# Kernel tuning notes

Measured on AMD Instinct MI355X. Metric: run time of the kernel, lower is better.

## Reference

```python
import jax, jax.numpy as jnp
import numpy as np

E = 1024  # embed_dim
H = 16    # num_heads
D = E // H  # head_dim


def setup_inputs() -> dict:
    key = jax.random.key(0)
    ks = jax.random.split(key, 9)
    s = 0.02
    return {
        "hidden_state": jax.random.normal(ks[0], (4, 1024, E), jnp.float32),
        "Wq": jax.random.normal(ks[1], (H, D, E), jnp.float32) * s,
        "bq": jax.random.normal(ks[2], (H, D), jnp.float32) * s,
        "Wk": jax.random.normal(ks[3], (H, D, E), jnp.float32) * s,
        "bk": jax.random.normal(ks[4], (H, D), jnp.float32) * s,
        "Wv": jax.random.normal(ks[5], (H, D, E), jnp.float32) * s,
        "bv": jax.random.normal(ks[6], (H, D), jnp.float32) * s,
        "Wo": jax.random.normal(ks[7], (E, E), jnp.float32) * s,
        "bo": jax.random.normal(ks[8], (E,), jnp.float32) * s,
    }


def _mha(x, Wq, bq, Wk, bk, Wv, bv, Wo, bo):
    # Per-head linear projections (torch Linear: y = x W^T + b), batched over heads.
    q = jnp.einsum("bse,hde->bhsd", x, Wq) + bq[None, :, None, :]
    k = jnp.einsum("bse,hde->bhsd", x, Wk) + bk[None, :, None, :]
    v = jnp.einsum("bse,hde->bhsd", x, Wv) + bv[None, :, None, :]
    scores = jnp.einsum("bhsd,bhtd->bhst", q, k) / jnp.sqrt(jnp.asarray(D, x.dtype))
    w = jax.nn.softmax(scores, axis=-1)  # F.softmax default -> last dim
    o = jnp.einsum("bhst,bhtd->bhsd", w, v)
    # concat heads along last dim: [B,S,H*D] in head order (matches torch.cat)
    B, _, S, _ = o.shape
    o = jnp.transpose(o, (0, 2, 1, 3)).reshape(B, S, H * D)
    return o @ Wo.T + bo


def reference(hidden_state, Wq, bq, Wk, bk, Wv, bv, Wo, bo):
    return _mha(hidden_state, Wq, bq, Wk, bk, Wv, bv, Wo, bo)
```

## Files before the change

kernel.cpp:

```cpp
#include <hip/hip_runtime.h>
#include <hip/hip_bf16.h>
#include <stdint.h>

#define E_DIM 1024
#define H_NUM 16
#define D_DIM 64
#define B_NUM 4
#define S_LEN 1024

typedef __attribute__((ext_vector_type(8))) short bf16x8;
typedef __attribute__((ext_vector_type(4))) short bf16x4;
typedef __attribute__((ext_vector_type(4))) float f32x4;

__device__ inline ushort f2b(float x) {
    __hip_bfloat16 h = __float2bfloat16(x);
    return *(ushort*)&h;
}
__device__ inline uint pk2(float a, float b) {
    __hip_bfloat162 h = __float22bfloat162_rn(make_float2(a, b));
    return *(uint*)&h;
}

__device__ inline void gld16(const ushort* g, ushort* l) {
    __builtin_amdgcn_global_load_lds((const __attribute__((address_space(1))) void*)g,
                                     (__attribute__((address_space(3))) void*)l, 16, 0, 0);
}

__global__ __launch_bounds__(256)
void convert_all(const float* __restrict__ X,  const float* __restrict__ Wq,
                 const float* __restrict__ Wk, const float* __restrict__ Wv,
                 const float* __restrict__ Wo,
                 ushort* __restrict__ Xb, ushort* __restrict__ Wcat,
                 ushort* __restrict__ Wob)
{
    const int bid = blockIdx.x;
    const float* src; ushort* dst; size_t off;
    if (bid < 4096)      { src = X;  dst = Xb;   off = (size_t)bid * 1024; }
    else if (bid < 5120) { src = Wq; dst = Wcat;              off = (size_t)(bid - 4096) * 1024; }
    else if (bid < 6144) { src = Wk; dst = Wcat + (1u << 20); off = (size_t)(bid - 5120) * 1024; }
    else if (bid < 7168) { src = Wv; dst = Wcat + (2u << 20); off = (size_t)(bid - 6144) * 1024; }
    else                 { src = Wo; dst = Wob;               off = (size_t)(bid - 7168) * 1024; }
    const size_t i = off + (size_t)threadIdx.x * 4;
    float4 v = *(const float4*)&src[i];
    ushort4 o;
    o.x = f2b(v.x); o.y = f2b(v.y); o.z = f2b(v.z); o.w = f2b(v.w);
    *(ushort4*)&dst[i] = o;
}

template<int MODE>
__global__ __launch_bounds__(256)
void gemm128(const ushort* __restrict__ A, const ushort* __restrict__ Bw,
             const float* __restrict__ b0, const float* __restrict__ b1,
             const float* __restrict__ b2,
             ushort* __restrict__ Qb, ushort* __restrict__ Kb,
             ushort* __restrict__ Vt_g, float* __restrict__ Cout, int K)
{
    constexpr int BM = 128;
    constexpr int BN = (MODE == 0) ? 128 : 64;
    constexpr int MI = (MODE == 0) ? 4 : 2;
    constexpr int NI = 4;

    __shared__ ushort As[BM * 32];
    __shared__ ushort Bs[BN * 32];

    const int tid  = threadIdx.x;
    const int wave = tid >> 6;
    const int lane = tid & 63;
    const int quad = lane >> 4;
    const int l16  = lane & 15;
    const int wm   = (MODE == 0) ? (wave & 1) : wave;
    const int wn   = (MODE == 0) ? (wave >> 1) : 0;
    const int moff = wm * MI * 16;
    const int noff = wn * NI * 16;
    const int m0   = blockIdx.x * BM;
    const int n0   = blockIdx.y * BN;

    f32x4 acc[MI][NI] = {};

    for (int k0 = 0; k0 < K; k0 += 32) {
#pragma unroll
        for (int i = 0; i < BM / 64; ++i) {
            const int e = i * 256 + tid;
            gld16(&A[(size_t)(m0 + (e >> 2)) * K + k0 + (e & 3) * 8], &As[e * 8]);
        }
#pragma unroll
        for (int i = 0; i < BN / 64; ++i) {
            const int e = i * 256 + tid;
            gld16(&Bw[(size_t)(n0 + (e >> 2)) * K + k0 + (e & 3) * 8], &Bs[e * 8]);
        }
        __syncthreads();

        bf16x8 af[MI], bf[NI];
#pragma unroll
        for (int mi = 0; mi < MI; ++mi)
            af[mi] = *(const bf16x8*)&As[(moff + mi * 16 + l16) * 32 + quad * 8];
#pragma unroll
        for (int ni = 0; ni < NI; ++ni)
            bf[ni] = *(const bf16x8*)&Bs[(noff + ni * 16 + l16) * 32 + quad * 8];
#pragma unroll
        for (int mi = 0; mi < MI; ++mi)
#pragma unroll
            for (int ni = 0; ni < NI; ++ni)
                acc[mi][ni] = __builtin_amdgcn_mfma_f32_16x16x32_bf16(af[mi], bf[ni], acc[mi][ni], 0, 0, 0);
        __syncthreads();
    }

    if (MODE == 0) {
        const int seg = n0 >> 10;
        const float* bp = (seg == 0) ? b0 : (seg == 1) ? b1 : b2;
        if (seg < 2) {
            ushort* dst = (seg == 0) ? Qb : Kb;
#pragma unroll
            for (int ni = 0; ni < NI; ++ni) {
                const int c = (n0 + noff + ni * 16 + l16) & 1023;
                const float bv = bp[c];
#pragma unroll
                for (int mi = 0; mi < MI; ++mi)
#pragma unroll
                    for (int r = 0; r < 4; ++r) {
                        const int m = m0 + moff + mi * 16 + quad * 4 + r;
                        dst[(size_t)m * 1024 + c] = f2b(acc[mi][ni][r] + bv);
                    }
            }
        } else {
#pragma unroll
            for (int ni = 0; ni < NI; ++ni) {
                const int c  = (n0 + noff + ni * 16 + l16) & 1023;
                const int hh = c >> 6, d = c & 63;
                const float bv = bp[c];
#pragma unroll
                for (int mi = 0; mi < MI; ++mi) {
                    const int mb = m0 + moff + mi * 16 + quad * 4;
                    const int b  = mb >> 10, s = mb & 1023;
                    ushort4 pk;
                    pk.x = f2b(acc[mi][ni][0] + bv);
                    pk.y = f2b(acc[mi][ni][1] + bv);
                    pk.z = f2b(acc[mi][ni][2] + bv);
                    pk.w = f2b(acc[mi][ni][3] + bv);
                    *(ushort4*)&Vt_g[(((size_t)(b * 16 + hh)) * 64 + d) * 1024 + s] = pk;
                }
            }
        }
    } else {
#pragma unroll
        for (int ni = 0; ni < NI; ++ni) {
            const int n = n0 + noff + ni * 16 + l16;
            const float bv = b0[n];
#pragma unroll
            for (int mi = 0; mi < MI; ++mi)
#pragma unroll
                for (int r = 0; r < 4; ++r) {
                    const int m = m0 + moff + mi * 16 + quad * 4 + r;
                    Cout[(size_t)m * 1024 + n] = acc[mi][ni][r] + bv;
                }
        }
    }
}

__global__ __launch_bounds__(256)
void attention3(const ushort* __restrict__ Qg, const ushort* __restrict__ Kg,
                const ushort* __restrict__ Vg, ushort* __restrict__ Og)
{
    __shared__ ushort Qs[64][72];
    __shared__ ushort Ks[64][72];
    __shared__ ushort Vt[64][72];

    const int tid  = threadIdx.x;
    const int w    = tid >> 6;
    const int lane = tid & 63;
    const int quad = lane >> 4;
    const int l16  = lane & 15;

    const int qt = blockIdx.x;
    const int bh = blockIdx.y;
    const int b  = bh >> 4;
    const int h  = bh & 15;
    const size_t tbase = ((size_t)b * S_LEN) * E_DIM + (size_t)h * D_DIM;
    const size_t vbase = (size_t)bh * D_DIM * S_LEN;

#pragma unroll
    for (int rr = 0; rr < 64; rr += 32) {
        const int r  = rr + (tid >> 3);
        const int c8 = (tid & 7) * 8;
        *(uint4*)&Qs[r][c8] = *(const uint4*)&Qg[tbase + (size_t)(qt * 64 + r) * E_DIM + c8];
    }
    __syncthreads();

    bf16x8 qf[2];
    qf[0] = *(const bf16x8*)&Qs[w * 16 + l16][quad * 8];
    qf[1] = *(const bf16x8*)&Qs[w * 16 + l16][32 + quad * 8];

    float lq = 0.0f;
    f32x4 oacc[4] = {};
    const float C2 = 0.18033688011f;

    for (int kt = 0; kt < 16; ++kt) {
        __syncthreads();
#pragma unroll
        for (int rr = 0; rr < 64; rr += 32) {
            const int r  = rr + (tid >> 3);
            const int c8 = (tid & 7) * 8;
            *(uint4*)&Ks[r][c8] = *(const uint4*)&Kg[tbase + (size_t)(kt * 64 + r) * E_DIM + c8];
            *(uint4*)&Vt[r][c8] = *(const uint4*)&Vg[vbase + (size_t)r * S_LEN + kt * 64 + c8];
        }
        __syncthreads();

        f32x4 sacc[4] = {};
#pragma unroll
        for (int mt = 0; mt < 4; ++mt)
#pragma unroll
            for (int ks = 0; ks < 2; ++ks) {
                bf16x8 kf = *(const bf16x8*)&Ks[mt * 16 + l16][ks * 32 + quad * 8];
                sacc[mt] = __builtin_amdgcn_mfma_f32_16x16x32_bf16(kf, qf[ks], sacc[mt], 0, 0, 0);
            }

        float p[4][4], rs = 0.0f;
#pragma unroll
        for (int mt = 0; mt < 4; ++mt)
#pragma unroll
            for (int r = 0; r < 4; ++r) {
                p[mt][r] = exp2f(sacc[mt][r] * C2);
                rs += p[mt][r];
            }
        lq += rs;

        bf16x4 pf[4];
#pragma unroll
        for (int kb = 0; kb < 4; ++kb) {
            union { uint u[2]; bf16x4 v; } pk;
            pk.u[0] = pk2(p[kb][0], p[kb][1]);
            pk.u[1] = pk2(p[kb][2], p[kb][3]);
            pf[kb] = pk.v;
        }

#pragma unroll
        for (int nb = 0; nb < 4; ++nb)
#pragma unroll
            for (int kb = 0; kb < 4; ++kb) {
                bf16x4 vf = *(const bf16x4*)&Vt[nb * 16 + l16][kb * 16 + quad * 4];
                oacc[nb] = __builtin_amdgcn_mfma_f32_16x16x16bf16_1k(pf[kb], vf, oacc[nb], 0, 0, 0);
            }
    }

    lq += __shfl_xor(lq, 16);
    lq += __shfl_xor(lq, 32);
    const float linv = 1.0f / lq;
    float lC[4];
#pragma unroll
    for (int r = 0; r < 4; ++r) lC[r] = __shfl(linv, quad * 4 + r);
#pragma unroll
    for (int nb = 0; nb < 4; ++nb)
#pragma unroll
        for (int r = 0; r < 4; ++r) {
            const int q = qt * 64 + w * 16 + quad * 4 + r;
            const int d = nb * 16 + l16;
            Og[tbase + (size_t)q * E_DIM + d] = f2b(oacc[nb][r] * lC[r]);
        }
}

extern "C" void kernel_launch(void* const* d_in, const int* in_sizes, int n_in,
                              void* d_out, int out_size, void* d_ws, size_t ws_size,
                              hipStream_t stream)
{
    (void)in_sizes; (void)n_in; (void)out_size; (void)ws_size;

    const float* X  = (const float*)d_in[0];
    const float* Wq = (const float*)d_in[1];
    const float* bq = (const float*)d_in[2];
    const float* Wk = (const float*)d_in[3];
    const float* bk = (const float*)d_in[4];
    const float* Wv = (const float*)d_in[5];
    const float* bv = (const float*)d_in[6];
    const float* Wo = (const float*)d_in[7];
    const float* bo = (const float*)d_in[8];

    const size_t MEG = 1u << 20;
    ushort* ws   = (ushort*)d_ws;
    ushort* Xb   = ws;
    ushort* Wcat = ws + 4 * MEG;
    ushort* Wob  = ws + 7 * MEG;
    ushort* Qb   = ws + 8 * MEG;
    ushort* Kb   = ws + 12 * MEG;
    ushort* Vtg  = ws + 16 * MEG;
    ushort* AO   = Xb;

    dim3 blk(256);

    convert_all<<<8192, blk, 0, stream>>>(X, Wq, Wk, Wv, Wo, Xb, Wcat, Wob);

    gemm128<0><<<dim3(32, 24), blk, 0, stream>>>(Xb, Wcat, bq, bk, bv,
                                                 Qb, Kb, Vtg, nullptr, E_DIM);

    attention3<<<dim3(16, 64), blk, 0, stream>>>(Qb, Kb, Vtg, AO);

    gemm128<1><<<dim3(32, 16), blk, 0, stream>>>(AO, Wob, bo, nullptr, nullptr,
                                                 nullptr, nullptr, nullptr,
                                                 (float*)d_out, E_DIM);
}
```

Before: 209.0 us.

## Double-buffer GEMM LDS tiles and prefetch attention K/V tiles into registers

```diff
diff --git a/kernel.cpp b/kernel.cpp
--- a/kernel.cpp
+++ b/kernel.cpp
@@ -60,8 +60,8 @@
     constexpr int MI = (MODE == 0) ? 4 : 2;
     constexpr int NI = 4;
 
-    __shared__ ushort As[BM * 32];
-    __shared__ ushort Bs[BN * 32];
+    __shared__ ushort As[2][BM * 32];
+    __shared__ ushort Bs[2][BN * 32];
 
     const int tid  = threadIdx.x;
     const int wave = tid >> 6;
@@ -77,26 +77,42 @@
 
     f32x4 acc[MI][NI] = {};
 
-    for (int k0 = 0; k0 < K; k0 += 32) {
-#pragma unroll
-        for (int i = 0; i < BM / 64; ++i) {
-            const int e = i * 256 + tid;
-            gld16(&A[(size_t)(m0 + (e >> 2)) * K + k0 + (e & 3) * 8], &As[e * 8]);
-        }
-#pragma unroll
-        for (int i = 0; i < BN / 64; ++i) {
-            const int e = i * 256 + tid;
-            gld16(&Bw[(size_t)(n0 + (e >> 2)) * K + k0 + (e & 3) * 8], &Bs[e * 8]);
-        }
-        __syncthreads();
+#pragma unroll
+    for (int i = 0; i < BM / 64; ++i) {
+        const int e = i * 256 + tid;
+        gld16(&A[(size_t)(m0 + (e >> 2)) * K + (e & 3) * 8], &As[0][e * 8]);
+    }
+#pragma unroll
+    for (int i = 0; i < BN / 64; ++i) {
+        const int e = i * 256 + tid;
+        gld16(&Bw[(size_t)(n0 + (e >> 2)) * K + (e & 3) * 8], &Bs[0][e * 8]);
+    }
+    __syncthreads();
+
+    const int nk = K >> 5;
+    for (int ki = 0; ki < nk; ++ki) {
+        const int cur = ki & 1;
+        if (ki + 1 < nk) {
+            const int k0 = (ki + 1) << 5;
+#pragma unroll
+            for (int i = 0; i < BM / 64; ++i) {
+                const int e = i * 256 + tid;
+                gld16(&A[(size_t)(m0 + (e >> 2)) * K + k0 + (e & 3) * 8], &As[cur ^ 1][e * 8]);
+            }
+#pragma unroll
+            for (int i = 0; i < BN / 64; ++i) {
+                const int e = i * 256 + tid;
+                gld16(&Bw[(size_t)(n0 + (e >> 2)) * K + k0 + (e & 3) * 8], &Bs[cur ^ 1][e * 8]);
+            }
+        }
 
         bf16x8 af[MI], bf[NI];
 #pragma unroll
         for (int mi = 0; mi < MI; ++mi)
-            af[mi] = *(const bf16x8*)&As[(moff + mi * 16 + l16) * 32 + quad * 8];
+            af[mi] = *(const bf16x8*)&As[cur][(moff + mi * 16 + l16) * 32 + quad * 8];
 #pragma unroll
         for (int ni = 0; ni < NI; ++ni)
-            bf[ni] = *(const bf16x8*)&Bs[(noff + ni * 16 + l16) * 32 + quad * 8];
+            bf[ni] = *(const bf16x8*)&Bs[cur][(noff + ni * 16 + l16) * 32 + quad * 8];
 #pragma unroll
         for (int mi = 0; mi < MI; ++mi)
 #pragma unroll
@@ -158,12 +174,10 @@
 }
 
 __global__ __launch_bounds__(256)
-void attention3(const ushort* __restrict__ Qg, const ushort* __restrict__ Kg,
+void attention4(const ushort* __restrict__ Qg, const ushort* __restrict__ Kg,
                 const ushort* __restrict__ Vg, ushort* __restrict__ Og)
 {
-    __shared__ ushort Qs[64][72];
-    __shared__ ushort Ks[64][72];
-    __shared__ ushort Vt[64][72];
+    __shared__ ushort S[4][64][68];
 
     const int tid  = threadIdx.x;
     const int w    = tid >> 6;
@@ -178,39 +192,46 @@
     const size_t tbase = ((size_t)b * S_LEN) * E_DIM + (size_t)h * D_DIM;
     const size_t vbase = (size_t)bh * D_DIM * S_LEN;
 
-#pragma unroll
-    for (int rr = 0; rr < 64; rr += 32) {
-        const int r  = rr + (tid >> 3);
-        const int c8 = (tid & 7) * 8;
-        *(uint4*)&Qs[r][c8] = *(const uint4*)&Qg[tbase + (size_t)(qt * 64 + r) * E_DIM + c8];
+    const int sr = tid >> 3;
+    const int c8 = (tid & 7) * 8;
+
+#pragma unroll
+    for (int g = 0; g < 2; ++g) {
+        const int rr = sr + g * 32;
+        *(uint4*)&S[2][rr][c8] = *(const uint4*)&Qg[tbase + (size_t)(qt * 64 + rr) * E_DIM + c8];
+        *(uint4*)&S[0][rr][c8] = *(const uint4*)&Kg[tbase + (size_t)rr * E_DIM + c8];
+        *(uint4*)&S[1][rr][c8] = *(const uint4*)&Vg[vbase + (size_t)rr * S_LEN + c8];
     }
     __syncthreads();
 
     bf16x8 qf[2];
-    qf[0] = *(const bf16x8*)&Qs[w * 16 + l16][quad * 8];
-    qf[1] = *(const bf16x8*)&Qs[w * 16 + l16][32 + quad * 8];
+    qf[0] = *(const bf16x8*)&S[2][w * 16 + l16][quad * 8];
+    qf[1] = *(const bf16x8*)&S[2][w * 16 + l16][32 + quad * 8];
+    __syncthreads();
 
     float lq = 0.0f;
     f32x4 oacc[4] = {};
     const float C2 = 0.18033688011f;
 
     for (int kt = 0; kt < 16; ++kt) {
-        __syncthreads();
-#pragma unroll
-        for (int rr = 0; rr < 64; rr += 32) {
-            const int r  = rr + (tid >> 3);
-            const int c8 = (tid & 7) * 8;
-            *(uint4*)&Ks[r][c8] = *(const uint4*)&Kg[tbase + (size_t)(kt * 64 + r) * E_DIM + c8];
-            *(uint4*)&Vt[r][c8] = *(const uint4*)&Vg[vbase + (size_t)r * S_LEN + kt * 64 + c8];
-        }
-        __syncthreads();
+        const int cur = kt & 1;
+
+        uint4 kpre[2], vpre[2];
+        if (kt < 15) {
+#pragma unroll
+            for (int g = 0; g < 2; ++g) {
+                const int rr = sr + g * 32;
+                kpre[g] = *(const uint4*)&Kg[tbase + (size_t)((kt + 1) * 64 + rr) * E_DIM + c8];
+                vpre[g] = *(const uint4*)&Vg[vbase + (size_t)rr * S_LEN + (kt + 1) * 64 + c8];
+            }
+        }
 
         f32x4 sacc[4] = {};
 #pragma unroll
         for (int mt = 0; mt < 4; ++mt)
 #pragma unroll
             for (int ks = 0; ks < 2; ++ks) {
-                bf16x8 kf = *(const bf16x8*)&Ks[mt * 16 + l16][ks * 32 + quad * 8];
+                bf16x8 kf = *(const bf16x8*)&S[cur * 2][mt * 16 + l16][ks * 32 + quad * 8];
                 sacc[mt] = __builtin_amdgcn_mfma_f32_16x16x32_bf16(kf, qf[ks], sacc[mt], 0, 0, 0);
             }
 
@@ -237,9 +258,20 @@
         for (int nb = 0; nb < 4; ++nb)
 #pragma unroll
             for (int kb = 0; kb < 4; ++kb) {
-                bf16x4 vf = *(const bf16x4*)&Vt[nb * 16 + l16][kb * 16 + quad * 4];
+                bf16x4 vf = *(const bf16x4*)&S[cur * 2 + 1][nb * 16 + l16][kb * 16 + quad * 4];
                 oacc[nb] = __builtin_amdgcn_mfma_f32_16x16x16bf16_1k(pf[kb], vf, oacc[nb], 0, 0, 0);
             }
+
+        if (kt < 15) {
+            const int nxt = cur ^ 1;
+#pragma unroll
+            for (int g = 0; g < 2; ++g) {
+                const int rr = sr + g * 32;
+                *(uint4*)&S[nxt * 2][rr][c8]     = kpre[g];
+                *(uint4*)&S[nxt * 2 + 1][rr][c8] = vpre[g];
+            }
+        }
+        __syncthreads();
     }
 
     lq += __shfl_xor(lq, 16);
@@ -291,7 +323,7 @@
     gemm128<0><<<dim3(32, 24), blk, 0, stream>>>(Xb, Wcat, bq, bk, bv,
                                                  Qb, Kb, Vtg, nullptr, E_DIM);
 
-    attention3<<<dim3(16, 64), blk, 0, stream>>>(Qb, Kb, Vtg, AO);
+    attention4<<<dim3(16, 64), blk, 0, stream>>>(Qb, Kb, Vtg, AO);
 
     gemm128<1><<<dim3(32, 16), blk, 0, stream>>>(AO, Wob, bo, nullptr, nullptr,
                                                  nullptr, nullptr, nullptr,
```

After: 203.0 us. 1.03x faster.
